# Optimization experiments

Measured on AMD Instinct MI355X. Metric: run time of the kernel, lower is better.

Reference implementation:

```python
import jax, jax.numpy as jnp
import numpy as np

DEPTH = 3
MAX_NB = 10

def setup_inputs() -> dict:
    key = jax.random.key(0)
    ks = jax.random.split(key, 10)
    B, N, NB, A, E, H = 64, 512, 600, 89, 5, 256
    input_atom = jax.random.normal(ks[0], (B, N, A), dtype=jnp.float32)
    input_bond = jax.random.normal(ks[1], (B, NB, E), dtype=jnp.float32)
    batch_idx = jnp.broadcast_to(jnp.arange(B, dtype=jnp.int32)[:, None, None], (B, N, MAX_NB))
    atom_nei = jax.random.randint(ks[2], (B, N, MAX_NB), 0, N, dtype=jnp.int32)
    bond_nei = jax.random.randint(ks[3], (B, N, MAX_NB), 0, NB, dtype=jnp.int32)
    atom_graph = jnp.stack([batch_idx, atom_nei], axis=-1)  # [B,N,MAX_NB,2]
    bond_graph = jnp.stack([batch_idx, bond_nei], axis=-1)
    num_nbs = jax.random.randint(ks[4], (B, N), 1, MAX_NB + 1, dtype=jnp.int32)
    s = 0.01
    W_atom = s * jax.random.normal(ks[5], (A, H), dtype=jnp.float32)
    W_U2 = s * jax.random.normal(ks[6], (H + E, H), dtype=jnp.float32)
    b_U2 = jnp.zeros((H,), dtype=jnp.float32)
    W_U1 = s * jax.random.normal(ks[7], (2 * H, H), dtype=jnp.float32)
    b_U1 = jnp.zeros((H,), dtype=jnp.float32)
    return {"input_atom": input_atom, "input_bond": input_bond,
            "atom_graph": atom_graph, "bond_graph": bond_graph, "num_nbs": num_nbs,
            "W_atom": W_atom, "W_U2": W_U2, "b_U2": b_U2, "W_U1": W_U1, "b_U1": b_U1}

def reference(input_atom, input_bond, atom_graph, bond_graph, num_nbs,
              W_atom, W_U2, b_U2, W_U1, b_U1):
    # atom embedding: [B,N,H]
    atom_features = input_atom @ W_atom
    # neighbor validity mask [B,N,MAX_NB,1] (tf.sequence_mask)
    mask = (jnp.arange(MAX_NB)[None, None, :] < num_nbs[:, :, None]).astype(atom_features.dtype)[..., None]
    ab, ai = atom_graph[..., 0], atom_graph[..., 1]
    bb, bi = bond_graph[..., 0], bond_graph[..., 1]
    fbond_nei = input_bond[bb, bi]  # [B,N,MAX_NB,5], constant across depth
    for _ in range(DEPTH):
        fatom_nei = atom_features[ab, ai]  # gather_nd -> [B,N,MAX_NB,H]
        l_nei = jnp.concatenate([fatom_nei, fbond_nei], axis=-1)  # [B,N,MAX_NB,H+5]
        pre_label = jax.nn.relu(l_nei @ W_U2 + b_U2)
        nei_label = jnp.sum(pre_label * mask, axis=-2)  # [B,N,H]
        new_label = jnp.concatenate([atom_features, nei_label], axis=-1)  # [B,N,2H]
        atom_features = jax.nn.relu(new_label @ W_U1 + b_U1)
    return atom_features
```

## Files before the change

### kernel.cpp

```cpp
#include <hip/hip_runtime.h>

constexpr int Bb   = 64;
constexpr int Nn   = 512;
constexpr int NBb  = 600;
constexpr int Ad   = 89;
constexpr int Ed   = 5;
constexpr int Hd   = 256;
constexpr int MNB  = 10;
constexpr int Mrows  = Bb * Nn;
constexpr int NBrows = Bb * NBb;
constexpr int Kpad   = 96;

typedef __bf16 bf16x8 __attribute__((ext_vector_type(8)));
typedef float  f32x4  __attribute__((ext_vector_type(4)));

typedef __attribute__((address_space(1))) const void gvoid_t;
typedef __attribute__((address_space(3))) void lvoid_t;

__device__ inline ushort bf_rne(float x) {
  unsigned u = __float_as_uint(x);
  unsigned r = (u + 0x7fffu + ((u >> 16) & 1u)) >> 16;
  return (ushort)r;
}
__device__ inline float bf_f(ushort h) { return __uint_as_float(((unsigned)h) << 16); }

constexpr int S0 = Mrows * Kpad / 256;
constexpr int S1 = NBrows / 8;
constexpr int S2 = Mrows * MNB / 256;
constexpr int S3 = 256;
constexpr int S4L = Hd * Kpad / 256;

__global__ __launch_bounds__(256)
void megaprep(const float* __restrict__ input_atom, const float* __restrict__ input_bond,
              const int* __restrict__ atom_graph, const int* __restrict__ bond_graph,
              const float* __restrict__ W_atom, const float* __restrict__ W_U2,
              const float* __restrict__ b_U2, const float* __restrict__ W_U1,
              ushort* __restrict__ Apadh, ushort* __restrict__ Z, uint* __restrict__ PIdx,
              ushort* __restrict__ w2h, ushort* __restrict__ w1ah, ushort* __restrict__ w1bh,
              ushort* __restrict__ wah) {
  const int blk = blockIdx.x;
  const int tid = threadIdx.x;
  if (blk < S0) {
    const int e = blk * 256 + tid;
    const int m = e / Kpad, c = e - m * Kpad;
    Apadh[e] = bf_rne(c < Ad ? input_atom[(size_t)m * Ad + c] : 0.f);
  } else if (blk < S0 + S1) {
    const int r0 = (blk - S0) * 8;
    const int h = tid;
    float w[Ed];
#pragma unroll
    for (int e = 0; e < Ed; ++e) w[e] = W_U2[(size_t)(Hd + e) * Hd + h];
    const float b2 = b_U2[h];
#pragma unroll
    for (int j = 0; j < 8; ++j) {
      const int r = r0 + j;
      const float* bp = input_bond + (size_t)r * Ed;
      float d = b2;
#pragma unroll
      for (int e = 0; e < Ed; ++e) d = fmaf(bp[e], w[e], d);
      Z[(size_t)r * Hd + h] = bf_rne(d);
    }
  } else if (blk < S0 + S1 + S2) {
    const int i = (blk - S0 - S1) * 256 + tid;
    const uint ai = (uint)atom_graph[(size_t)i * 2 + 1];
    const uint bi = (uint)bond_graph[(size_t)i * 2 + 1];
    PIdx[i] = (ai << 16) | bi;
  } else if (blk < S0 + S1 + S2 + S3) {
    const int n = blk - S0 - S1 - S2;
    const int k = tid;
    const size_t o = (size_t)n * 256 + k;
    w2h[o]  = bf_rne(W_U2[(size_t)k * Hd + n]);
    w1ah[o] = bf_rne(W_U1[(size_t)k * Hd + n]);
    w1bh[o] = bf_rne(W_U1[(size_t)(k + 256) * Hd + n]);
  } else {
    const int e = (blk - S0 - S1 - S2 - S3) * 256 + tid;
    const int n = e / Kpad, k = e - n * Kpad;
    wah[e] = bf_rne((k < Ad) ? W_atom[(size_t)k * Hd + n] : 0.f);
  }
}

struct TUSegs { const ushort* a[2]; const ushort* bt[2]; const ushort* bp[2]; };

template<int NSEG, int KD>
__global__ __launch_bounds__(256)
void gemm_tu(TUSegs segs, const float* __restrict__ bias,
             ushort* __restrict__ Tout, ushort* __restrict__ Pout) {
  constexpr int NK = KD / 32;
  constexpr int TS = NSEG * NK;
  __shared__ ushort As[2][4096];
  __shared__ ushort Bt[2][4096];
  __shared__ ushort Bp[2][4096];
  const int tid  = threadIdx.x;
  const int lane = tid & 63;
  const int w    = tid >> 6;
  const int wr   = w >> 1, wc = w & 1;
  const int m0   = blockIdx.x * 128;
  const int n0   = blockIdx.y * 128;
  const int arow = tid >> 2;
  const int acol = (tid & 3) * 8;
  const int fr   = lane & 15;
  const int fq   = lane >> 4;

  f32x4 accT[4][4] = {};
  f32x4 accP[4][4] = {};

  auto stage = [&](const ushort* Aseg, const ushort* Bts, const ushort* Bps,
                   int kk, int db) {
#pragma unroll
    for (int i = 0; i < 2; ++i) {
      const ushort* ga = Aseg + (size_t)(m0 + arow + 64 * i) * KD + kk + acol;
      __builtin_amdgcn_global_load_lds((gvoid_t*)ga,
          (lvoid_t*)(&As[db][i * 2048 + w * 512]), 16, 0, 0);
      const ushort* gt = Bts + (size_t)(n0 + arow + 64 * i) * KD + kk + acol;
      __builtin_amdgcn_global_load_lds((gvoid_t*)gt,
          (lvoid_t*)(&Bt[db][i * 2048 + w * 512]), 16, 0, 0);
      const ushort* gp = Bps + (size_t)(n0 + arow + 64 * i) * KD + kk + acol;
      __builtin_amdgcn_global_load_lds((gvoid_t*)gp,
          (lvoid_t*)(&Bp[db][i * 2048 + w * 512]), 16, 0, 0);
    }
  };

  stage(segs.a[0], segs.bt[0], segs.bp[0], 0, 0);
  __syncthreads();

#pragma unroll
  for (int ts = 0; ts < TS; ++ts) {
    const int db = ts & 1;
    if (ts + 1 < TS) {
      const int s2 = (ts + 1) / NK;
      const int k2 = (ts + 1) % NK;
      stage(segs.a[s2], segs.bt[s2], segs.bp[s2], k2 * 32, db ^ 1);
    }
    bf16x8 bt_[4], bp_[4];
#pragma unroll
    for (int nf = 0; nf < 4; ++nf) {
      bt_[nf] = *reinterpret_cast<const bf16x8*>(&Bt[db][(wc * 64 + nf * 16 + fr) * 32 + fq * 8]);
      bp_[nf] = *reinterpret_cast<const bf16x8*>(&Bp[db][(wc * 64 + nf * 16 + fr) * 32 + fq * 8]);
    }
#pragma unroll
    for (int mf = 0; mf < 4; ++mf) {
      bf16x8 af = *reinterpret_cast<const bf16x8*>(&As[db][(wr * 64 + mf * 16 + fr) * 32 + fq * 8]);
#pragma unroll
      for (int nf = 0; nf < 4; ++nf) {
        accT[mf][nf] = __builtin_amdgcn_mfma_f32_16x16x32_bf16(af, bt_[nf], accT[mf][nf], 0, 0, 0);
        accP[mf][nf] = __builtin_amdgcn_mfma_f32_16x16x32_bf16(af, bp_[nf], accP[mf][nf], 0, 0, 0);
      }
    }
    __syncthreads();
  }

#pragma unroll
  for (int mf = 0; mf < 4; ++mf) {
#pragma unroll
    for (int nf = 0; nf < 4; ++nf) {
      const int col = n0 + wc * 64 + nf * 16 + fr;
      const float bv = bias[col];
#pragma unroll
      for (int r = 0; r < 4; ++r) {
        const int row = m0 + wr * 64 + mf * 16 + fq * 4 + r;
        Tout[(size_t)row * Hd + col] = bf_rne(accT[mf][nf][r]);
        Pout[(size_t)row * Hd + col] = bf_rne(accP[mf][nf][r] + bv);
      }
    }
  }
}

struct SegPtrs { const ushort* a[2]; const ushort* b[2]; };

template<int NSEG, int KD, int OUTMODE, bool RELU, bool BIAS, bool CLOAD>
__global__ __launch_bounds__(256)
void gemm_mfma(SegPtrs segs, const float* __restrict__ bias,
               const ushort* __restrict__ Pin,
               float* __restrict__ Cf, ushort* __restrict__ Chi) {
  constexpr int NK = KD / 32;
  constexpr int TS = NSEG * NK;
  __shared__ ushort As[2][4096];
  __shared__ ushort Bs[2][4096];
  const int tid  = threadIdx.x;
  const int lane = tid & 63;
  const int w    = tid >> 6;
  const int wr   = w >> 1, wc = w & 1;
  const int m0   = blockIdx.x * 128;
  const int n0   = blockIdx.y * 128;
  const int arow = tid >> 2;
  const int acol = (tid & 3) * 8;
  const int fr   = lane & 15;
  const int fq   = lane >> 4;

  f32x4 acc[4][4] = {};

  auto stage = [&](const ushort* Aseg, const ushort* Bseg, int kk, int db) {
#pragma unroll
    for (int i = 0; i < 2; ++i) {
      const ushort* ga = Aseg + (size_t)(m0 + arow + 64 * i) * KD + kk + acol;
      const ushort* gb = Bseg + (size_t)(n0 + arow + 64 * i) * KD + kk + acol;
      __builtin_amdgcn_global_load_lds((gvoid_t*)ga,
          (lvoid_t*)(&As[db][i * 2048 + w * 512]), 16, 0, 0);
      __builtin_amdgcn_global_load_lds((gvoid_t*)gb,
          (lvoid_t*)(&Bs[db][i * 2048 + w * 512]), 16, 0, 0);
    }
  };

  stage(segs.a[0], segs.b[0], 0, 0);
  __syncthreads();

#pragma unroll
  for (int ts = 0; ts < TS; ++ts) {
    const int db = ts & 1;
    if (ts + 1 < TS) {
      const int s2 = (ts + 1) / NK;
      const int k2 = (ts + 1) % NK;
      stage(segs.a[s2], segs.b[s2], k2 * 32, db ^ 1);
    }
    bf16x8 bfr[4];
#pragma unroll
    for (int nf = 0; nf < 4; ++nf)
      bfr[nf] = *reinterpret_cast<const bf16x8*>(&Bs[db][(wc * 64 + nf * 16 + fr) * 32 + fq * 8]);
#pragma unroll
    for (int mf = 0; mf < 4; ++mf) {
      bf16x8 af = *reinterpret_cast<const bf16x8*>(&As[db][(wr * 64 + mf * 16 + fr) * 32 + fq * 8]);
#pragma unroll
      for (int nf = 0; nf < 4; ++nf)
        acc[mf][nf] = __builtin_amdgcn_mfma_f32_16x16x32_bf16(af, bfr[nf], acc[mf][nf], 0, 0, 0);
    }
    __syncthreads();
  }

#pragma unroll
  for (int mf = 0; mf < 4; ++mf) {
#pragma unroll
    for (int nf = 0; nf < 4; ++nf) {
      const int col = n0 + wc * 64 + nf * 16 + fr;
      float bv = 0.f;
      if constexpr (BIAS) bv = bias[col];
#pragma unroll
      for (int r = 0; r < 4; ++r) {
        const int row = m0 + wr * 64 + mf * 16 + fq * 4 + r;
        float v = acc[mf][nf][r] + bv;
        if constexpr (CLOAD) v += bf_f(Pin[(size_t)row * Hd + col]);
        if constexpr (RELU) v = fmaxf(v, 0.f);
        const size_t o = (size_t)row * Hd + col;
        if constexpr (OUTMODE == 0) Cf[o] = v;
        else                        Chi[o] = bf_rne(v);
      }
    }
  }
}

__global__ __launch_bounds__(256)
void nei_z(const ushort* __restrict__ T, const ushort* __restrict__ Z,
           const uint* __restrict__ PIdx, const int* __restrict__ num_nbs,
           ushort* __restrict__ NEI) {
  const int ho = threadIdx.x & 31;
  const int rp = threadIdx.x >> 5;
  int bid = blockIdx.x;
  bid = (bid & 7) * (gridDim.x >> 3) + (bid >> 3);
  const int m = bid * 8 + rp;
  const int b = m >> 9;
  const int h0 = ho * 8;
  const int nn = num_nbs[m];

  uint pk[MNB];
#pragma unroll
  for (int q = 0; q < 5; ++q) {
    const uint2 u = *reinterpret_cast<const uint2*>(&PIdx[(size_t)m * MNB + q * 2]);
    pk[q * 2] = u.x; pk[q * 2 + 1] = u.y;
  }
  int ai[MNB], bi[MNB];
#pragma unroll
  for (int k = 0; k < MNB; ++k) { ai[k] = (int)(pk[k] >> 16); bi[k] = (int)(pk[k] & 0xffffu); }
#pragma unroll
  for (int k = 1; k < MNB; ++k) {
    ai[k] = (k < nn) ? ai[k] : ai[0];
    bi[k] = (k < nn) ? bi[k] : bi[0];
  }

  float acc[8] = {};
#pragma unroll
  for (int ch = 0; ch < 2; ++ch) {
    uint4 tv[5], zv[5];
#pragma unroll
    for (int k5 = 0; k5 < 5; ++k5) {
      const int k = ch * 5 + k5;
      tv[k5] = *reinterpret_cast<const uint4*>(&T[(((size_t)b << 9) + ai[k]) * Hd + h0]);
      zv[k5] = *reinterpret_cast<const uint4*>(&Z[((size_t)b * NBb + bi[k]) * Hd + h0]);
    }
#pragma unroll
    for (int k5 = 0; k5 < 5; ++k5) {
      const int k = ch * 5 + k5;
      const uint tw[4] = {tv[k5].x, tv[k5].y, tv[k5].z, tv[k5].w};
      const uint zw[4] = {zv[k5].x, zv[k5].y, zv[k5].z, zv[k5].w};
      if (k < nn) {
#pragma unroll
        for (int q = 0; q < 4; ++q) {
          acc[q * 2]     += fmaxf(__uint_as_float(tw[q] << 16) + __uint_as_float(zw[q] << 16), 0.f);
          acc[q * 2 + 1] += fmaxf(__uint_as_float(tw[q] & 0xffff0000u) + __uint_as_float(zw[q] & 0xffff0000u), 0.f);
        }
      }
    }
  }
  uint4 o;
  o.x = (uint)bf_rne(acc[0]) | ((uint)bf_rne(acc[1]) << 16);
  o.y = (uint)bf_rne(acc[2]) | ((uint)bf_rne(acc[3]) << 16);
  o.z = (uint)bf_rne(acc[4]) | ((uint)bf_rne(acc[5]) << 16);
  o.w = (uint)bf_rne(acc[6]) | ((uint)bf_rne(acc[7]) << 16);
  *reinterpret_cast<uint4*>(&NEI[(size_t)m * Hd + h0]) = o;
}

extern "C" void kernel_launch(void* const* d_in, const int* in_sizes, int n_in,
                              void* d_out, int out_size, void* d_ws, size_t ws_size,
                              hipStream_t stream) {
  const float* input_atom = (const float*)d_in[0];
  const float* input_bond = (const float*)d_in[1];
  const int*   atom_graph = (const int*)d_in[2];
  const int*   bond_graph = (const int*)d_in[3];
  const int*   num_nbs    = (const int*)d_in[4];
  const float* W_atom     = (const float*)d_in[5];
  const float* W_U2       = (const float*)d_in[6];
  const float* b_U2       = (const float*)d_in[7];
  const float* W_U1       = (const float*)d_in[8];
  const float* b_U1       = (const float*)d_in[9];

  const size_t SL = (size_t)Mrows * Hd;
  ushort* AFa  = (ushort*)d_ws;
  ushort* AFb  = AFa + SL;
  uint*   PIdx = (uint*)(AFb + SL);
  ushort* w2h  = (ushort*)(PIdx + (size_t)Mrows * MNB);
  ushort* w1ah = w2h  + 256 * 256;
  ushort* w1bh = w1ah + 256 * 256;
  ushort* wah  = w1bh + 256 * 256;
  ushort* Apadh= wah  + Hd * Kpad;
  ushort* Zbuf = Apadh + (size_t)Mrows * Kpad;

  ushort* Tbf = (ushort*)d_out;
  ushort* Pbf = Tbf + SL;

  const dim3 blk(256);
  const dim3 gG(Mrows / 128, Hd / 128);

  megaprep<<<S0 + S1 + S2 + S3 + S4L, blk, 0, stream>>>(
      input_atom, input_bond, atom_graph, bond_graph, W_atom, W_U2, b_U2, W_U1,
      Apadh, Zbuf, PIdx, w2h, w1ah, w1bh, wah);

  {
    SegPtrs se{};
    se.a[0] = Apadh;
    se.b[0] = wah;
    gemm_mfma<1, Kpad, 2, false, false, false><<<gG, blk, 0, stream>>>(se, nullptr, nullptr, nullptr, AFa);
  }

  for (int d = 0; d < 2; ++d) {
    TUSegs t{};
    t.a[0] = AFa; t.bt[0] = w2h; t.bp[0] = w1ah;
    gemm_tu<1, Hd><<<gG, blk, 0, stream>>>(t, b_U1, Tbf, Pbf);

    nei_z<<<Mrows / 8, blk, 0, stream>>>(Tbf, Zbuf, PIdx, num_nbs, AFb);

    SegPtrs s{};
    s.a[0] = AFb; s.b[0] = w1bh;
    gemm_mfma<1, Hd, 2, true, false, true><<<gG, blk, 0, stream>>>(s, nullptr, Pbf, nullptr, AFa);
  }

  {
    SegPtrs s{};
    s.a[0] = AFa; s.b[0] = w2h;
    gemm_mfma<1, Hd, 2, false, false, false><<<gG, blk, 0, stream>>>(s, nullptr, nullptr, nullptr, Tbf);
  }
  nei_z<<<Mrows / 8, blk, 0, stream>>>(Tbf, Zbuf, PIdx, num_nbs, AFb);
  {
    SegPtrs s{};
    s.a[0] = AFa; s.a[1] = AFb;
    s.b[0] = w1ah; s.b[1] = w1bh;
    gemm_mfma<2, Hd, 0, true, true, false><<<gG, blk, 0, stream>>>(s, b_U1, nullptr, (float*)d_out, nullptr);
  }
}
```

Baseline: 179.7 us.

## Fuse neighbor gather-sum into the following U1 GEMM as its A-operand producer

Removes the separate nei_z kernel and the NEI intermediate buffer. The neighbor gather, relu and masked sum are computed directly into the GEMM's shared-memory A tile. The new kernel uses 128-row blocks covering the full 256-column output with 512 threads, so each row's gather runs exactly once per stage. This saves a global write and read of the neighbor tensor and one launch per depth. The cost is gather latency inside the GEMM pipeline, only 256 blocks instead of 512, and larger per-block register and LDS use.

Measured after the change: 211.1 us. 1.17x slower.

```diff
diff --git a/kernel.cpp b/kernel.cpp
--- a/kernel.cpp
+++ b/kernel.cpp
@@ -167,11 +167,9 @@
 
 struct SegPtrs { const ushort* a[2]; const ushort* b[2]; };
 
-template<int NSEG, int KD, int OUTMODE, bool RELU, bool BIAS, bool CLOAD>
+template<int NSEG, int KD>
 __global__ __launch_bounds__(256)
-void gemm_mfma(SegPtrs segs, const float* __restrict__ bias,
-               const ushort* __restrict__ Pin,
-               float* __restrict__ Cf, ushort* __restrict__ Chi) {
+void gemm_mfma(SegPtrs segs, ushort* __restrict__ Chi) {
   constexpr int NK = KD / 32;
   constexpr int TS = NSEG * NK;
   __shared__ ushort As[2][4096];
@@ -231,80 +229,144 @@
 #pragma unroll
     for (int nf = 0; nf < 4; ++nf) {
       const int col = n0 + wc * 64 + nf * 16 + fr;
-      float bv = 0.f;
-      if constexpr (BIAS) bv = bias[col];
 #pragma unroll
       for (int r = 0; r < 4; ++r) {
         const int row = m0 + wr * 64 + mf * 16 + fq * 4 + r;
-        float v = acc[mf][nf][r] + bv;
-        if constexpr (CLOAD) v += bf_f(Pin[(size_t)row * Hd + col]);
-        if constexpr (RELU) v = fmaxf(v, 0.f);
-        const size_t o = (size_t)row * Hd + col;
-        if constexpr (OUTMODE == 0) Cf[o] = v;
-        else                        Chi[o] = bf_rne(v);
-      }
-    }
-  }
-}
-
-__global__ __launch_bounds__(256)
-void nei_z(const ushort* __restrict__ T, const ushort* __restrict__ Z,
-           const uint* __restrict__ PIdx, const int* __restrict__ num_nbs,
-           ushort* __restrict__ NEI) {
-  const int ho = threadIdx.x & 31;
-  const int rp = threadIdx.x >> 5;
-  int bid = blockIdx.x;
-  bid = (bid & 7) * (gridDim.x >> 3) + (bid >> 3);
-  const int m = bid * 8 + rp;
-  const int b = m >> 9;
-  const int h0 = ho * 8;
-  const int nn = num_nbs[m];
-
-  uint pk[MNB];
-#pragma unroll
-  for (int q = 0; q < 5; ++q) {
-    const uint2 u = *reinterpret_cast<const uint2*>(&PIdx[(size_t)m * MNB + q * 2]);
-    pk[q * 2] = u.x; pk[q * 2 + 1] = u.y;
-  }
-  int ai[MNB], bi[MNB];
-#pragma unroll
-  for (int k = 0; k < MNB; ++k) { ai[k] = (int)(pk[k] >> 16); bi[k] = (int)(pk[k] & 0xffffu); }
-#pragma unroll
-  for (int k = 1; k < MNB; ++k) {
-    ai[k] = (k < nn) ? ai[k] : ai[0];
-    bi[k] = (k < nn) ? bi[k] : bi[0];
-  }
-
-  float acc[8] = {};
-#pragma unroll
-  for (int ch = 0; ch < 2; ++ch) {
-    uint4 tv[5], zv[5];
-#pragma unroll
-    for (int k5 = 0; k5 < 5; ++k5) {
-      const int k = ch * 5 + k5;
-      tv[k5] = *reinterpret_cast<const uint4*>(&T[(((size_t)b << 9) + ai[k]) * Hd + h0]);
-      zv[k5] = *reinterpret_cast<const uint4*>(&Z[((size_t)b * NBb + bi[k]) * Hd + h0]);
-    }
-#pragma unroll
-    for (int k5 = 0; k5 < 5; ++k5) {
-      const int k = ch * 5 + k5;
-      const uint tw[4] = {tv[k5].x, tv[k5].y, tv[k5].z, tv[k5].w};
-      const uint zw[4] = {zv[k5].x, zv[k5].y, zv[k5].z, zv[k5].w};
-      if (k < nn) {
-#pragma unroll
-        for (int q = 0; q < 4; ++q) {
-          acc[q * 2]     += fmaxf(__uint_as_float(tw[q] << 16) + __uint_as_float(zw[q] << 16), 0.f);
-          acc[q * 2 + 1] += fmaxf(__uint_as_float(tw[q] & 0xffff0000u) + __uint_as_float(zw[q] & 0xffff0000u), 0.f);
+        Chi[(size_t)row * Hd + col] = bf_rne(acc[mf][nf][r]);
+      }
+    }
+  }
+}
+
+template<bool FINAL>
+__global__ __launch_bounds__(512)
+void gemm_nei(const ushort* __restrict__ T, const ushort* __restrict__ Z,
+              const uint* __restrict__ PIdx, const int* __restrict__ num_nbs,
+              const ushort* __restrict__ w1b,
+              const ushort* __restrict__ AF, const ushort* __restrict__ w1a,
+              const ushort* __restrict__ Pin, const float* __restrict__ bias,
+              float* __restrict__ Cf, ushort* __restrict__ Chi) {
+  __shared__ ushort As[2][128 * 32];
+  __shared__ ushort Bs[2][256 * 32];
+  __shared__ uint   pkL[128 * MNB];
+  __shared__ int    nnL[128];
+  const int tid  = threadIdx.x;
+  const int lane = tid & 63;
+  const int w    = tid >> 6;
+  const int wr   = w >> 1, wc = w & 1;
+  const int m0   = blockIdx.x * 128;
+  const int fr   = lane & 15;
+  const int fq   = lane >> 4;
+  const int b    = m0 >> 9;
+  const size_t tb = ((size_t)b << 9) * Hd;
+  const size_t zb = (size_t)b * NBb * Hd;
+
+  for (int i = tid; i < 128 * MNB; i += 512) pkL[i] = PIdx[(size_t)m0 * MNB + i];
+  if (tid < 128) nnL[tid] = num_nbs[m0 + tid];
+  __syncthreads();
+
+  f32x4 acc[2][8] = {};
+
+  auto stageB = [&](const ushort* Bp, int kk, int db) {
+#pragma unroll
+    for (int i = 0; i < 2; ++i) {
+      const ushort* g = Bp + (size_t)((tid >> 2) + 128 * i) * Hd + kk + (tid & 3) * 8;
+      __builtin_amdgcn_global_load_lds((gvoid_t*)g,
+          (lvoid_t*)(&Bs[db][i * 4096 + w * 512]), 16, 0, 0);
+    }
+  };
+  auto stageA_normal = [&](const ushort* Ap, int kk, int db) {
+    const ushort* g = Ap + (size_t)(m0 + (tid >> 2)) * Hd + kk + (tid & 3) * 8;
+    __builtin_amdgcn_global_load_lds((gvoid_t*)g,
+        (lvoid_t*)(&As[db][w * 512]), 16, 0, 0);
+  };
+  auto stageA_gather = [&](int kk, int db) {
+    const int row  = tid >> 2;
+    const int ch   = tid & 3;
+    const int nn   = nnL[row];
+    const int koff = kk + ch * 8;
+    float a[8] = {};
+#pragma unroll
+    for (int h5 = 0; h5 < 2; ++h5) {
+      uint4 tv[5], zv[5];
+#pragma unroll
+      for (int j5 = 0; j5 < 5; ++j5) {
+        const int j = h5 * 5 + j5;
+        uint pk = pkL[row * MNB + j];
+        pk = (j < nn) ? pk : pkL[row * MNB];
+        tv[j5] = *reinterpret_cast<const uint4*>(&T[tb + (size_t)(pk >> 16) * Hd + koff]);
+        zv[j5] = *reinterpret_cast<const uint4*>(&Z[zb + (size_t)(pk & 0xffffu) * Hd + koff]);
+      }
+#pragma unroll
+      for (int j5 = 0; j5 < 5; ++j5) {
+        const int j = h5 * 5 + j5;
+        const uint tw[4] = {tv[j5].x, tv[j5].y, tv[j5].z, tv[j5].w};
+        const uint zw[4] = {zv[j5].x, zv[j5].y, zv[j5].z, zv[j5].w};
+        if (j < nn) {
+#pragma unroll
+          for (int q = 0; q < 4; ++q) {
+            a[q * 2]     += fmaxf(__uint_as_float(tw[q] << 16) + __uint_as_float(zw[q] << 16), 0.f);
+            a[q * 2 + 1] += fmaxf(__uint_as_float(tw[q] & 0xffff0000u) + __uint_as_float(zw[q] & 0xffff0000u), 0.f);
+          }
         }
       }
     }
-  }
-  uint4 o;
-  o.x = (uint)bf_rne(acc[0]) | ((uint)bf_rne(acc[1]) << 16);
-  o.y = (uint)bf_rne(acc[2]) | ((uint)bf_rne(acc[3]) << 16);
-  o.z = (uint)bf_rne(acc[4]) | ((uint)bf_rne(acc[5]) << 16);
-  o.w = (uint)bf_rne(acc[6]) | ((uint)bf_rne(acc[7]) << 16);
-  *reinterpret_cast<uint4*>(&NEI[(size_t)m * Hd + h0]) = o;
+    uint4 o;
+    o.x = (uint)bf_rne(a[0]) | ((uint)bf_rne(a[1]) << 16);
+    o.y = (uint)bf_rne(a[2]) | ((uint)bf_rne(a[3]) << 16);
+    o.z = (uint)bf_rne(a[4]) | ((uint)bf_rne(a[5]) << 16);
+    o.w = (uint)bf_rne(a[6]) | ((uint)bf_rne(a[7]) << 16);
+    *reinterpret_cast<uint4*>(&As[db][row * 32 + ch * 8]) = o;
+  };
+
+  constexpr int TS = FINAL ? 16 : 8;
+  if constexpr (FINAL) { stageA_normal(AF, 0, 0); stageB(w1a, 0, 0); }
+  else                 { stageA_gather(0, 0);     stageB(w1b, 0, 0); }
+  __syncthreads();
+
+#pragma unroll
+  for (int ts = 0; ts < TS; ++ts) {
+    const int db = ts & 1;
+    if (ts + 1 < TS) {
+      const int t2 = ts + 1;
+      if constexpr (FINAL) {
+        if (t2 < 8) { stageA_normal(AF, t2 * 32, db ^ 1); stageB(w1a, t2 * 32, db ^ 1); }
+        else        { stageA_gather((t2 - 8) * 32, db ^ 1); stageB(w1b, (t2 - 8) * 32, db ^ 1); }
+      } else {
+        stageA_gather(t2 * 32, db ^ 1); stageB(w1b, t2 * 32, db ^ 1);
+      }
+    }
+    bf16x8 bfr[8];
+#pragma unroll
+    for (int nf = 0; nf < 8; ++nf)
+      bfr[nf] = *reinterpret_cast<const bf16x8*>(&Bs[db][(wc * 128 + nf * 16 + fr) * 32 + fq * 8]);
+#pragma unroll
+    for (int mf = 0; mf < 2; ++mf) {
+      bf16x8 af = *reinterpret_cast<const bf16x8*>(&As[db][(wr * 32 + mf * 16 + fr) * 32 + fq * 8]);
+#pragma unroll
+      for (int nf = 0; nf < 8; ++nf)
+        acc[mf][nf] = __builtin_amdgcn_mfma_f32_16x16x32_bf16(af, bfr[nf], acc[mf][nf], 0, 0, 0);
+    }
+    __syncthreads();
+  }
+
+#pragma unroll
+  for (int mf = 0; mf < 2; ++mf) {
+#pragma unroll
+    for (int nf = 0; nf < 8; ++nf) {
+      const int col = wc * 128 + nf * 16 + fr;
+#pragma unroll
+      for (int r = 0; r < 4; ++r) {
+        const int row = m0 + wr * 32 + mf * 16 + fq * 4 + r;
+        if constexpr (FINAL) {
+          Cf[(size_t)row * Hd + col] = fmaxf(acc[mf][nf][r] + bias[col], 0.f);
+        } else {
+          const float v = fmaxf(acc[mf][nf][r] + bf_f(Pin[(size_t)row * Hd + col]), 0.f);
+          Chi[(size_t)row * Hd + col] = bf_rne(v);
+        }
+      }
+    }
+  }
 }
 
 extern "C" void kernel_launch(void* const* d_in, const int* in_sizes, int n_in,
@@ -332,11 +394,11 @@
   ushort* Apadh= wah  + Hd * Kpad;
   ushort* Zbuf = Apadh + (size_t)Mrows * Kpad;
 
-  ushort* Tbf = (ushort*)d_out;
-  ushort* Pbf = Tbf + SL;
+  ushort* Pbf = (ushort*)d_out + SL;
 
   const dim3 blk(256);
   const dim3 gG(Mrows / 128, Hd / 128);
+  const dim3 gN(Mrows / 128, 1);
 
   megaprep<<<S0 + S1 + S2 + S3 + S4L, blk, 0, stream>>>(
       input_atom, input_bond, atom_graph, bond_graph, W_atom, W_U2, b_U2, W_U1,
@@ -344,33 +406,26 @@
 
   {
     SegPtrs se{};
-    se.a[0] = Apadh;
-    se.b[0] = wah;
-    gemm_mfma<1, Kpad, 2, false, false, false><<<gG, blk, 0, stream>>>(se, nullptr, nullptr, nullptr, AFa);
+    se.a[0] = Apadh; se.b[0] = wah;
+    gemm_mfma<1, Kpad><<<gG, blk, 0, stream>>>(se, AFa);
   }
 
   for (int d = 0; d < 2; ++d) {
     TUSegs t{};
     t.a[0] = AFa; t.bt[0] = w2h; t.bp[0] = w1ah;
-    gemm_tu<1, Hd><<<gG, blk, 0, stream>>>(t, b_U1, Tbf, Pbf);
-
-    nei_z<<<Mrows / 8, blk, 0, stream>>>(Tbf, Zbuf, PIdx, num_nbs, AFb);
-
-    SegPtrs s{};
-    s.a[0] = AFb; s.b[0] = w1bh;
-    gemm_mfma<1, Hd, 2, true, false, true><<<gG, blk, 0, stream>>>(s, nullptr, Pbf, nullptr, AFa);
+    gemm_tu<1, Hd><<<gG, blk, 0, stream>>>(t, b_U1, AFb, Pbf);
+
+    gemm_nei<false><<<gN, 512, 0, stream>>>(AFb, Zbuf, PIdx, num_nbs, w1bh,
+                                            nullptr, nullptr, Pbf, nullptr,
+                                            nullptr, AFa);
   }
 
   {
     SegPtrs s{};
     s.a[0] = AFa; s.b[0] = w2h;
-    gemm_mfma<1, Hd, 2, false, false, false><<<gG, blk, 0, stream>>>(s, nullptr, nullptr, nullptr, Tbf);
-  }
-  nei_z<<<Mrows / 8, blk, 0, stream>>>(Tbf, Zbuf, PIdx, num_nbs, AFb);
-  {
-    SegPtrs s{};
-    s.a[0] = AFa; s.a[1] = AFb;
-    s.b[0] = w1ah; s.b[1] = w1bh;
-    gemm_mfma<2, Hd, 0, true, true, false><<<gG, blk, 0, stream>>>(s, b_U1, nullptr, (float*)d_out, nullptr);
-  }
-}
+    gemm_mfma<1, Hd><<<gG, blk, 0, stream>>>(s, AFb);
+  }
+  gemm_nei<true><<<gN, 512, 0, stream>>>(AFb, Zbuf, PIdx, num_nbs, w1bh,
+                                         AFa, w1ah, nullptr, b_U1,
+                                         (float*)d_out, nullptr);
+}
```

## Fold atom embedding into combined first-layer weights and widen N-tile for U1 GEMMs

Applied to the files above, without the earlier changes.

Precomputes W_atom·W_U2 and W_atom·W_U1a as small combined weight matrices, so the first iteration's T/P GEMM runs directly on the padded input atoms (K=96) instead of first materialising the atom embedding (K=256). This drops one full GEMM pass over the activations. It also adds a gemm_k2 kernel with 512 threads that covers all 256 output columns per block, so each A tile is loaded once rather than twice. Composing the weights in bf16 adds some rounding error.

Result: faster. 160.5 us (-10.7%).

```diff
diff --git a/kernel.cpp b/kernel.cpp
--- a/kernel.cpp
+++ b/kernel.cpp
@@ -28,7 +28,7 @@
 constexpr int S1 = NBrows / 8;
 constexpr int S2 = Mrows * MNB / 256;
 constexpr int S3 = 256;
-constexpr int S4L = Hd * Kpad / 256;
+constexpr int S4 = Kpad * Hd / 256;
 
 __global__ __launch_bounds__(256)
 void megaprep(const float* __restrict__ input_atom, const float* __restrict__ input_bond,
@@ -37,7 +37,7 @@
               const float* __restrict__ b_U2, const float* __restrict__ W_U1,
               ushort* __restrict__ Apadh, ushort* __restrict__ Z, uint* __restrict__ PIdx,
               ushort* __restrict__ w2h, ushort* __restrict__ w1ah, ushort* __restrict__ w1bh,
-              ushort* __restrict__ wah) {
+              ushort* __restrict__ wabf) {
   const int blk = blockIdx.x;
   const int tid = threadIdx.x;
   if (blk < S0) {
@@ -74,19 +74,87 @@
     w1bh[o] = bf_rne(W_U1[(size_t)(k + 256) * Hd + n]);
   } else {
     const int e = (blk - S0 - S1 - S2 - S3) * 256 + tid;
-    const int n = e / Kpad, k = e - n * Kpad;
-    wah[e] = bf_rne((k < Ad) ? W_atom[(size_t)k * Hd + n] : 0.f);
-  }
-}
-
-struct TUSegs { const ushort* a[2]; const ushort* bt[2]; const ushort* bp[2]; };
-
-template<int NSEG, int KD>
+    const int a = e >> 8, h = e & 255;
+    wabf[e] = bf_rne((a < Ad) ? W_atom[(size_t)a * Hd + h] : 0.f);
+  }
+}
+
 __global__ __launch_bounds__(256)
-void gemm_tu(TUSegs segs, const float* __restrict__ bias,
+void gemm_wcomb(const ushort* __restrict__ w2h, const ushort* __restrict__ w1ah,
+                const ushort* __restrict__ wabf,
+                ushort* __restrict__ wc2T, ushort* __restrict__ wc1T) {
+  __shared__ ushort As[2][4096];
+  __shared__ ushort Bs[2][4096];
+  const ushort* Apan = blockIdx.y ? w1ah : w2h;
+  ushort*       Cpan = blockIdx.y ? wc1T : wc2T;
+  const int tid  = threadIdx.x;
+  const int lane = tid & 63;
+  const int w    = tid >> 6;
+  const int wr   = w >> 1, wc = w & 1;
+  const int m0   = blockIdx.x * 128;
+  const int arow = tid >> 2;
+  const int acol = (tid & 3) * 8;
+  const int fr   = lane & 15;
+  const int fq   = lane >> 4;
+
+  f32x4 acc[4][4] = {};
+
+  auto stage = [&](int kk, int db) {
+#pragma unroll
+    for (int i = 0; i < 2; ++i) {
+      const ushort* ga = Apan + (size_t)(m0 + arow + 64 * i) * 256 + kk + acol;
+      __builtin_amdgcn_global_load_lds((gvoid_t*)ga,
+          (lvoid_t*)(&As[db][i * 2048 + w * 512]), 16, 0, 0);
+      const int brow = min(arow + 64 * i, Kpad - 1);
+      const ushort* gb = wabf + (size_t)brow * 256 + kk + acol;
+      __builtin_amdgcn_global_load_lds((gvoid_t*)gb,
+          (lvoid_t*)(&Bs[db][i * 2048 + w * 512]), 16, 0, 0);
+    }
+  };
+
+  stage(0, 0);
+  __syncthreads();
+
+#pragma unroll
+  for (int ts = 0; ts < 8; ++ts) {
+    const int db = ts & 1;
+    if (ts + 1 < 8) stage((ts + 1) * 32, db ^ 1);
+    bf16x8 bfr[4];
+#pragma unroll
+    for (int nf = 0; nf < 4; ++nf)
+      bfr[nf] = *reinterpret_cast<const bf16x8*>(&Bs[db][(wc * 64 + nf * 16 + fr) * 32 + fq * 8]);
+#pragma unroll
+    for (int mf = 0; mf < 4; ++mf) {
+      bf16x8 af = *reinterpret_cast<const bf16x8*>(&As[db][(wr * 64 + mf * 16 + fr) * 32 + fq * 8]);
+#pragma unroll
+      for (int nf = 0; nf < 4; ++nf)
+        acc[mf][nf] = __builtin_amdgcn_mfma_f32_16x16x32_bf16(af, bfr[nf], acc[mf][nf], 0, 0, 0);
+    }
+    __syncthreads();
+  }
+
+#pragma unroll
+  for (int mf = 0; mf < 4; ++mf) {
+#pragma unroll
+    for (int nf = 0; nf < 4; ++nf) {
+      const int col = wc * 64 + nf * 16 + fr;
+      if (col < Kpad) {
+#pragma unroll
+        for (int r = 0; r < 4; ++r) {
+          const int row = m0 + wr * 64 + mf * 16 + fq * 4 + r;
+          Cpan[(size_t)row * Kpad + col] = bf_rne(acc[mf][nf][r]);
+        }
+      }
+    }
+  }
+}
+
+template<int KD>
+__global__ __launch_bounds__(256)
+void gemm_tu(const ushort* __restrict__ A, const ushort* __restrict__ Bt_,
+             const ushort* __restrict__ Bp_, const float* __restrict__ bias,
              ushort* __restrict__ Tout, ushort* __restrict__ Pout) {
-  constexpr int NK = KD / 32;
-  constexpr int TS = NSEG * NK;
+  constexpr int TS = KD / 32;
   __shared__ ushort As[2][4096];
   __shared__ ushort Bt[2][4096];
   __shared__ ushort Bp[2][4096];
@@ -104,33 +172,28 @@
   f32x4 accT[4][4] = {};
   f32x4 accP[4][4] = {};
 
-  auto stage = [&](const ushort* Aseg, const ushort* Bts, const ushort* Bps,
-                   int kk, int db) {
+  auto stage = [&](int kk, int db) {
 #pragma unroll
     for (int i = 0; i < 2; ++i) {
-      const ushort* ga = Aseg + (size_t)(m0 + arow + 64 * i) * KD + kk + acol;
+      const ushort* ga = A + (size_t)(m0 + arow + 64 * i) * KD + kk + acol;
       __builtin_amdgcn_global_load_lds((gvoid_t*)ga,
           (lvoid_t*)(&As[db][i * 2048 + w * 512]), 16, 0, 0);
-      const ushort* gt = Bts + (size_t)(n0 + arow + 64 * i) * KD + kk + acol;
+      const ushort* gt = Bt_ + (size_t)(n0 + arow + 64 * i) * KD + kk + acol;
       __builtin_amdgcn_global_load_lds((gvoid_t*)gt,
           (lvoid_t*)(&Bt[db][i * 2048 + w * 512]), 16, 0, 0);
-      const ushort* gp = Bps + (size_t)(n0 + arow + 64 * i) * KD + kk + acol;
+      const ushort* gp = Bp_ + (size_t)(n0 + arow + 64 * i) * KD + kk + acol;
       __builtin_amdgcn_global_load_lds((gvoid_t*)gp,
           (lvoid_t*)(&Bp[db][i * 2048 + w * 512]), 16, 0, 0);
     }
   };
 
-  stage(segs.a[0], segs.bt[0], segs.bp[0], 0, 0);
+  stage(0, 0);
   __syncthreads();
 
 #pragma unroll
   for (int ts = 0; ts < TS; ++ts) {
     const int db = ts & 1;
-    if (ts + 1 < TS) {
-      const int s2 = (ts + 1) / NK;
-      const int k2 = (ts + 1) % NK;
-      stage(segs.a[s2], segs.bt[s2], segs.bp[s2], k2 * 32, db ^ 1);
-    }
+    if (ts + 1 < TS) stage((ts + 1) * 32, db ^ 1);
     bf16x8 bt_[4], bp_[4];
 #pragma unroll
     for (int nf = 0; nf < 4; ++nf) {
@@ -165,15 +228,9 @@
   }
 }
 
-struct SegPtrs { const ushort* a[2]; const ushort* b[2]; };
-
-template<int NSEG, int KD, int OUTMODE, bool RELU, bool BIAS, bool CLOAD>
 __global__ __launch_bounds__(256)
-void gemm_mfma(SegPtrs segs, const float* __restrict__ bias,
-               const ushort* __restrict__ Pin,
-               float* __restrict__ Cf, ushort* __restrict__ Chi) {
-  constexpr int NK = KD / 32;
-  constexpr int TS = NSEG * NK;
+void gemm_t(const ushort* __restrict__ A, const ushort* __restrict__ B,
+            ushort* __restrict__ Chi) {
   __shared__ ushort As[2][4096];
   __shared__ ushort Bs[2][4096];
   const int tid  = threadIdx.x;
@@ -189,11 +246,11 @@
 
   f32x4 acc[4][4] = {};
 
-  auto stage = [&](const ushort* Aseg, const ushort* Bseg, int kk, int db) {
+  auto stage = [&](int kk, int db) {
 #pragma unroll
     for (int i = 0; i < 2; ++i) {
-      const ushort* ga = Aseg + (size_t)(m0 + arow + 64 * i) * KD + kk + acol;
-      const ushort* gb = Bseg + (size_t)(n0 + arow + 64 * i) * KD + kk + acol;
+      const ushort* ga = A + (size_t)(m0 + arow + 64 * i) * Hd + kk + acol;
+      const ushort* gb = B + (size_t)(n0 + arow + 64 * i) * Hd + kk + acol;
       __builtin_amdgcn_global_load_lds((gvoid_t*)ga,
           (lvoid_t*)(&As[db][i * 2048 + w * 512]), 16, 0, 0);
       __builtin_amdgcn_global_load_lds((gvoid_t*)gb,
@@ -201,47 +258,118 @@
     }
   };
 
-  stage(segs.a[0], segs.b[0], 0, 0);
+  stage(0, 0);
+  __syncthreads();
+
+#pragma unroll
+  for (int ts = 0; ts < 8; ++ts) {
+    const int db = ts & 1;
+    if (ts + 1 < 8) stage((ts + 1) * 32, db ^ 1);
+    bf16x8 bfr[4];
+#pragma unroll
+    for (int nf = 0; nf < 4; ++nf)
+      bfr[nf] = *reinterpret_cast<const bf16x8*>(&Bs[db][(wc * 64 + nf * 16 + fr) * 32 + fq * 8]);
+#pragma unroll
+    for (int mf = 0; mf < 4; ++mf) {
+      bf16x8 af = *reinterpret_cast<const bf16x8*>(&As[db][(wr * 64 + mf * 16 + fr) * 32 + fq * 8]);
+#pragma unroll
+      for (int nf = 0; nf < 4; ++nf)
+        acc[mf][nf] = __builtin_amdgcn_mfma_f32_16x16x32_bf16(af, bfr[nf], acc[mf][nf], 0, 0, 0);
+    }
+    __syncthreads();
+  }
+
+#pragma unroll
+  for (int mf = 0; mf < 4; ++mf) {
+#pragma unroll
+    for (int nf = 0; nf < 4; ++nf) {
+      const int col = n0 + wc * 64 + nf * 16 + fr;
+#pragma unroll
+      for (int r = 0; r < 4; ++r) {
+        const int row = m0 + wr * 64 + mf * 16 + fq * 4 + r;
+        Chi[(size_t)row * Hd + col] = bf_rne(acc[mf][nf][r]);
+      }
+    }
+  }
+}
+
+template<bool FINAL>
+__global__ __launch_bounds__(512)
+void gemm_k2(const ushort* __restrict__ NEI, const ushort* __restrict__ w1b,
+             const ushort* __restrict__ AF, const ushort* __restrict__ w1a,
+             const ushort* __restrict__ Pin, const float* __restrict__ bias,
+             float* __restrict__ Cf, ushort* __restrict__ Chi) {
+  __shared__ ushort As[2][128 * 32];
+  __shared__ ushort Bs[2][256 * 32];
+  const int tid  = threadIdx.x;
+  const int lane = tid & 63;
+  const int w    = tid >> 6;
+  const int wr   = w >> 1, wc = w & 1;
+  const int m0   = blockIdx.x * 128;
+  const int fr   = lane & 15;
+  const int fq   = lane >> 4;
+
+  f32x4 acc[2][8] = {};
+
+  auto stageA = [&](const ushort* Ap, int kk, int db) {
+    const ushort* g = Ap + (size_t)(m0 + (tid >> 2)) * Hd + kk + (tid & 3) * 8;
+    __builtin_amdgcn_global_load_lds((gvoid_t*)g,
+        (lvoid_t*)(&As[db][w * 512]), 16, 0, 0);
+  };
+  auto stageB = [&](const ushort* Bp, int kk, int db) {
+#pragma unroll
+    for (int i = 0; i < 2; ++i) {
+      const ushort* g = Bp + (size_t)((tid >> 2) + 128 * i) * Hd + kk + (tid & 3) * 8;
+      __builtin_amdgcn_global_load_lds((gvoid_t*)g,
+          (lvoid_t*)(&Bs[db][i * 4096 + w * 512]), 16, 0, 0);
+    }
+  };
+
+  constexpr int TS = FINAL ? 16 : 8;
+  if constexpr (FINAL) { stageA(AF, 0, 0); stageB(w1a, 0, 0); }
+  else                 { stageA(NEI, 0, 0); stageB(w1b, 0, 0); }
   __syncthreads();
 
 #pragma unroll
   for (int ts = 0; ts < TS; ++ts) {
     const int db = ts & 1;
     if (ts + 1 < TS) {
-      const int s2 = (ts + 1) / NK;
-      const int k2 = (ts + 1) % NK;
-      stage(segs.a[s2], segs.b[s2], k2 * 32, db ^ 1);
-    }
-    bf16x8 bfr[4];
-#pragma unroll
-    for (int nf = 0; nf < 4; ++nf)
-      bfr[nf] = *reinterpret_cast<const bf16x8*>(&Bs[db][(wc * 64 + nf * 16 + fr) * 32 + fq * 8]);
-#pragma unroll
-    for (int mf = 0; mf < 4; ++mf) {
-      bf16x8 af = *reinterpret_cast<const bf16x8*>(&As[db][(wr * 64 + mf * 16 + fr) * 32 + fq * 8]);
-#pragma unroll
-      for (int nf = 0; nf < 4; ++nf)
+      const int t2 = ts + 1;
+      if constexpr (FINAL) {
+        if (t2 < 8) { stageA(AF, t2 * 32, db ^ 1); stageB(w1a, t2 * 32, db ^ 1); }
+        else        { stageA(NEI, (t2 - 8) * 32, db ^ 1); stageB(w1b, (t2 - 8) * 32, db ^ 1); }
+      } else {
+        stageA(NEI, t2 * 32, db ^ 1); stageB(w1b, t2 * 32, db ^ 1);
+      }
+    }
+    bf16x8 bfr[8];
+#pragma unroll
+    for (int nf = 0; nf < 8; ++nf)
+      bfr[nf] = *reinterpret_cast<const bf16x8*>(&Bs[db][(wc * 128 + nf * 16 + fr) * 32 + fq * 8]);
+#pragma unroll
+    for (int mf = 0; mf < 2; ++mf) {
+      bf16x8 af = *reinterpret_cast<const bf16x8*>(&As[db][(wr * 32 + mf * 16 + fr) * 32 + fq * 8]);
+#pragma unroll
+      for (int nf = 0; nf < 8; ++nf)
         acc[mf][nf] = __builtin_amdgcn_mfma_f32_16x16x32_bf16(af, bfr[nf], acc[mf][nf], 0, 0, 0);
     }
     __syncthreads();
   }
 
 #pragma unroll
-  for (int mf = 0; mf < 4; ++mf) {
-#pragma unroll
-    for (int nf = 0; nf < 4; ++nf) {
-      const int col = n0 + wc * 64 + nf * 16 + fr;
-      float bv = 0.f;
-      if constexpr (BIAS) bv = bias[col];
+  for (int mf = 0; mf < 2; ++mf) {
+#pragma unroll
+    for (int nf = 0; nf < 8; ++nf) {
+      const int col = wc * 128 + nf * 16 + fr;
 #pragma unroll
       for (int r = 0; r < 4; ++r) {
-        const int row = m0 + wr * 64 + mf * 16 + fq * 4 + r;
-        float v = acc[mf][nf][r] + bv;
-        if constexpr (CLOAD) v += bf_f(Pin[(size_t)row * Hd + col]);
-        if constexpr (RELU) v = fmaxf(v, 0.f);
-        const size_t o = (size_t)row * Hd + col;
-        if constexpr (OUTMODE == 0) Cf[o] = v;
-        else                        Chi[o] = bf_rne(v);
+        const int row = m0 + wr * 32 + mf * 16 + fq * 4 + r;
+        if constexpr (FINAL) {
+          Cf[(size_t)row * Hd + col] = fmaxf(acc[mf][nf][r] + bias[col], 0.f);
+        } else {
+          const float v = fmaxf(acc[mf][nf][r] + bf_f(Pin[(size_t)row * Hd + col]), 0.f);
+          Chi[(size_t)row * Hd + col] = bf_rne(v);
+        }
       }
     }
   }
@@ -328,8 +456,10 @@
   ushort* w2h  = (ushort*)(PIdx + (size_t)Mrows * MNB);
   ushort* w1ah = w2h  + 256 * 256;
   ushort* w1bh = w1ah + 256 * 256;
-  ushort* wah  = w1bh + 256 * 256;
-  ushort* Apadh= wah  + Hd * Kpad;
+  ushort* wabf = w1bh + 256 * 256;
+  ushort* wc2T = wabf + Kpad * Hd;
+  ushort* wc1T = wc2T + Hd * Kpad;
+  ushort* Apadh= wc1T + Hd * Kpad;
   ushort* Zbuf = Apadh + (size_t)Mrows * Kpad;
 
   ushort* Tbf = (ushort*)d_out;
@@ -337,40 +467,26 @@
 
   const dim3 blk(256);
   const dim3 gG(Mrows / 128, Hd / 128);
-
-  megaprep<<<S0 + S1 + S2 + S3 + S4L, blk, 0, stream>>>(
+  const dim3 gK(Mrows / 128, 1);
+
+  megaprep<<<S0 + S1 + S2 + S3 + S4, blk, 0, stream>>>(
       input_atom, input_bond, atom_graph, bond_graph, W_atom, W_U2, b_U2, W_U1,
-      Apadh, Zbuf, PIdx, w2h, w1ah, w1bh, wah);
-
-  {
-    SegPtrs se{};
-    se.a[0] = Apadh;
-    se.b[0] = wah;
-    gemm_mfma<1, Kpad, 2, false, false, false><<<gG, blk, 0, stream>>>(se, nullptr, nullptr, nullptr, AFa);
-  }
-
-  for (int d = 0; d < 2; ++d) {
-    TUSegs t{};
-    t.a[0] = AFa; t.bt[0] = w2h; t.bp[0] = w1ah;
-    gemm_tu<1, Hd><<<gG, blk, 0, stream>>>(t, b_U1, Tbf, Pbf);
-
-    nei_z<<<Mrows / 8, blk, 0, stream>>>(Tbf, Zbuf, PIdx, num_nbs, AFb);
-
-    SegPtrs s{};
-    s.a[0] = AFb; s.b[0] = w1bh;
-    gemm_mfma<1, Hd, 2, true, false, true><<<gG, blk, 0, stream>>>(s, nullptr, Pbf, nullptr, AFa);
-  }
-
-  {
-    SegPtrs s{};
-    s.a[0] = AFa; s.b[0] = w2h;
-    gemm_mfma<1, Hd, 2, false, false, false><<<gG, blk, 0, stream>>>(s, nullptr, nullptr, nullptr, Tbf);
-  }
+      Apadh, Zbuf, PIdx, w2h, w1ah, w1bh, wabf);
+
+  gemm_wcomb<<<dim3(2, 2), blk, 0, stream>>>(w2h, w1ah, wabf, wc2T, wc1T);
+
+  gemm_tu<Kpad><<<gG, blk, 0, stream>>>(Apadh, wc2T, wc1T, b_U1, Tbf, Pbf);
   nei_z<<<Mrows / 8, blk, 0, stream>>>(Tbf, Zbuf, PIdx, num_nbs, AFb);
-  {
-    SegPtrs s{};
-    s.a[0] = AFa; s.a[1] = AFb;
-    s.b[0] = w1ah; s.b[1] = w1bh;
-    gemm_mfma<2, Hd, 0, true, true, false><<<gG, blk, 0, stream>>>(s, b_U1, nullptr, (float*)d_out, nullptr);
-  }
-}
+  gemm_k2<false><<<gK, 512, 0, stream>>>(AFb, w1bh, nullptr, nullptr, Pbf,
+                                         nullptr, nullptr, AFa);
+
+  gemm_tu<Hd><<<gG, blk, 0, stream>>>(AFa, w2h, w1ah, b_U1, Tbf, Pbf);
+  nei_z<<<Mrows / 8, blk, 0, stream>>>(Tbf, Zbuf, PIdx, num_nbs, AFb);
+  gemm_k2<false><<<gK, 512, 0, stream>>>(AFb, w1bh, nullptr, nullptr, Pbf,
+                                         nullptr, nullptr, AFa);
+
+  gemm_t<<<gG, blk, 0, stream>>>(AFa, w2h, Tbf);
+  nei_z<<<Mrows / 8, blk, 0, stream>>>(Tbf, Zbuf, PIdx, num_nbs, AFb);
+  gemm_k2<true><<<gK, 512, 0, stream>>>(AFb, w1bh, AFa, w1ah, nullptr, b_U1,
+                                        (float*)d_out, nullptr);
+}
```
